# Kernel tuning notes

Hardware: AMD Instinct MI355X
Metric: run time of the kernel (lower is better)

## Reference

```python
import jax, jax.numpy as jnp
import numpy as np

REG_TOPK = 4
REG_CHANNELS = 64
ADD_MEAN = True
TOTAL_DIM = REG_TOPK + (1 if ADD_MEAN else 0)  # 5


def setup_inputs() -> dict:
    key = jax.random.key(0)
    k1, k2, k3 = jax.random.split(key, 3)
    N, C, H, W = 32, 32, 160, 160  # C = 4*(reg_max+1), reg_max=7
    x = jax.random.normal(k1, (N, C, H, W), dtype=jnp.float32)
    # 1x1 conv params, init std=0.01, bias 0 (as in torch module)
    w1 = jax.random.normal(k2, (REG_CHANNELS, 4 * TOTAL_DIM), dtype=jnp.float32) * 0.01
    b1 = jnp.zeros((REG_CHANNELS,), dtype=jnp.float32)
    w2 = jax.random.normal(k3, (1, REG_CHANNELS), dtype=jnp.float32) * 0.01
    b2 = jnp.zeros((1,), dtype=jnp.float32)
    return {"x": x, "w1": w1, "b1": b1, "w2": w2, "b2": b2}


def reference(x, w1, b1, w2, b2):
    N, C, H, W = x.shape
    bins = C // 4
    # softmax over distribution bins; move bins to last axis for top_k
    p = jax.nn.softmax(x.reshape(N, 4, bins, H, W), axis=2)  # (N,4,bins,H,W)
    p = jnp.transpose(p, (0, 1, 3, 4, 2))                    # (N,4,H,W,bins)
    topk, _ = jax.lax.top_k(p, REG_TOPK)                     # (N,4,H,W,k)
    if ADD_MEAN:
        stat = jnp.concatenate([topk, topk.mean(axis=-1, keepdims=True)], axis=-1)
    else:
        stat = topk                                          # (N,4,H,W,total_dim)
    # reshape to (N, 4*total_dim, H, W) matching torch layout (4, total_dim contiguous)
    stat = jnp.transpose(stat, (0, 1, 4, 2, 3)).reshape(N, 4 * TOTAL_DIM, H, W)
    y = jax.nn.relu(jnp.einsum('nchw,oc->nohw', stat, w1) + b1[None, :, None, None])
    y = jax.nn.sigmoid(jnp.einsum('nchw,oc->nohw', y, w2) + b2[None, :, None, None])
    return y
```

## Files before the change

kernel.cpp:

```cpp
#include <hip/hip_runtime.h>

#define HW_ 25600
#define CHW_ (32 * 25600)
#define NPIX 819200
#define ROWH 16

typedef _Float16 f16x8 __attribute__((ext_vector_type(8)));
typedef _Float16 h2 __attribute__((ext_vector_type(2)));
typedef float f32x4 __attribute__((ext_vector_type(4)));

__device__ __forceinline__ unsigned short h2us(_Float16 h) {
    return __builtin_bit_cast(unsigned short, h);
}
__device__ __forceinline__ unsigned packlo(h2 a, h2 b) {
    h2 r = {a.x, b.x};
    return __builtin_bit_cast(unsigned, r);
}
__device__ __forceinline__ unsigned packhi(h2 a, h2 b) {
    h2 r = {a.y, b.y};
    return __builtin_bit_cast(unsigned, r);
}
__device__ __forceinline__ h2 pkrtz(float a, float b) {
    return __builtin_bit_cast(h2, __builtin_amdgcn_cvt_pkrtz(a, b));
}

__global__ __launch_bounds__(256) void dgqp_fused(
    const float* __restrict__ x,
    const float* __restrict__ w1,
    const float* __restrict__ b1,
    const float* __restrict__ w2,
    const float* __restrict__ b2,
    float* __restrict__ out)
{
    __shared__ _Float16 smem[512 * ROWH + 2048];
    _Float16* sstats = smem;
    _Float16* swf    = smem + 512 * ROWH;

    const int tid  = threadIdx.x;
    const int lane = tid & 63;
    const int wpb  = (tid & 192) << 1;
    const int q    = lane & 15;
    const int kg   = lane >> 4;
    const int base = (blockIdx.x * 256 + tid) * 2;
    const unsigned int n = (unsigned int)base / HW_;
    const unsigned int off = (unsigned int)base + n * (unsigned int)(CHW_ - HW_);
    const float* xp = x + off;

    _Float16* row0 = sstats + (tid * 2) * ROWH;
    _Float16* row1 = row0 + ROWH;

#define PROC(g, buf) do {                                                    \
        h2 e[8];                                                             \
        _Pragma("unroll")                                                    \
        for (int b = 0; b < 8; ++b)                                          \
            e[b] = pkrtz(__expf(buf[b].x), __expf(buf[b].y));                \
        h2 t0 = (h2)0, t1 = (h2)0, t2 = (h2)0, t3 = (h2)0;                   \
        _Pragma("unroll")                                                    \
        for (int b = 0; b < 8; ++b) {                                        \
            h2 u0 = __builtin_elementwise_min(t0, e[b]);                     \
            t0    = __builtin_elementwise_max(t0, e[b]);                     \
            h2 u1 = __builtin_elementwise_min(t1, u0);                       \
            t1    = __builtin_elementwise_max(t1, u0);                       \
            h2 u2 = __builtin_elementwise_min(t2, u1);                       \
            t2    = __builtin_elementwise_max(t2, u1);                       \
            t3    = __builtin_elementwise_max(t3, u2);                       \
        }                                                                    \
        h2 sum = ((e[0] + e[1]) + (e[2] + e[3])) + ((e[4] + e[5]) + (e[6] + e[7])); \
        float ix = __builtin_amdgcn_rcpf((float)sum.x);                      \
        float iy = __builtin_amdgcn_rcpf((float)sum.y);                      \
        h2 inv = pkrtz(ix, iy);                                              \
        t0 = t0 * inv; t1 = t1 * inv; t2 = t2 * inv; t3 = t3 * inv;          \
        *reinterpret_cast<uint2*>(row0 + (g) * 4) =                          \
            make_uint2(packlo(t0, t1), packlo(t2, t3));                      \
        *reinterpret_cast<uint2*>(row1 + (g) * 4) =                          \
            make_uint2(packhi(t0, t1), packhi(t2, t3));                      \
    } while (0)

    float2 va[8], vb[8];
    #pragma unroll
    for (int b = 0; b < 8; ++b)
        va[b] = *reinterpret_cast<const float2*>(xp + (size_t)b * HW_);
    #pragma unroll
    for (int b = 0; b < 8; ++b)
        vb[b] = *reinterpret_cast<const float2*>(xp + (size_t)(8 + b) * HW_);
    __builtin_amdgcn_sched_barrier(0);
    PROC(0, va);
    #pragma unroll
    for (int b = 0; b < 8; ++b)
        va[b] = *reinterpret_cast<const float2*>(xp + (size_t)(16 + b) * HW_);
    __builtin_amdgcn_sched_barrier(0);
    PROC(1, vb);
    #pragma unroll
    for (int b = 0; b < 8; ++b)
        vb[b] = *reinterpret_cast<const float2*>(xp + (size_t)(24 + b) * HW_);
    __builtin_amdgcn_sched_barrier(0);
    PROC(2, va);
    __builtin_amdgcn_sched_barrier(0);
    PROC(3, vb);
#undef PROC

    {
        const int col = ((tid >> 6) << 4) | (tid & 15);
        const int kg2 = (tid >> 4) & 3;
        unsigned int pk[4];
        #pragma unroll
        for (int pr = 0; pr < 4; ++pr) {
            unsigned short hh[2];
            #pragma unroll
            for (int e = 0; e < 2; ++e) {
                int k = kg2 * 8 + pr * 2 + e;
                float v = 0.f;
                if (k < 16) {
                    int g = k >> 2, idx = k & 3;
                    v = w1[col * 20 + g * 5 + idx] + 0.25f * w1[col * 20 + g * 5 + 4];
                }
                hh[e] = h2us((_Float16)v);
            }
            pk[pr] = (unsigned int)hh[0] | ((unsigned int)hh[1] << 16);
        }
        *reinterpret_cast<uint4*>(swf + tid * 8) = make_uint4(pk[0], pk[1], pk[2], pk[3]);
    }
    __syncthreads();

    f16x8 wfrag[4];
    #pragma unroll
    for (int ct = 0; ct < 4; ++ct)
        wfrag[ct] = *reinterpret_cast<const f16x8*>(swf + (ct * 64 + lane) * 8);

    f32x4 w2v[4], b1c[4];
    #pragma unroll
    for (int ct = 0; ct < 4; ++ct) {
        w2v[ct] = *reinterpret_cast<const f32x4*>(w2 + ct * 16 + kg * 4);
        b1c[ct] = *reinterpret_cast<const f32x4*>(b1 + ct * 16 + kg * 4);
    }

    const float bb2 = b2[0];
    const int outbase = blockIdx.x * 512 + wpb;

    #pragma unroll
    for (int m = 0; m < 8; ++m) {
        f16x8 sfrag = *reinterpret_cast<const f16x8*>(
            sstats + (wpb + m * 16 + q) * ROWH + kg * 8);

        float pp = 0.f;
        #pragma unroll
        for (int ct = 0; ct < 4; ++ct) {
            f32x4 d = __builtin_amdgcn_mfma_f32_16x16x32_f16(wfrag[ct], sfrag, b1c[ct], 0, 0, 0);
            pp = fmaf(w2v[ct][0], fmaxf(d[0], 0.f), pp);
            pp = fmaf(w2v[ct][1], fmaxf(d[1], 0.f), pp);
            pp = fmaf(w2v[ct][2], fmaxf(d[2], 0.f), pp);
            pp = fmaf(w2v[ct][3], fmaxf(d[3], 0.f), pp);
        }
        pp += __shfl_xor(pp, 16);
        pp += __shfl_xor(pp, 32);
        float y = __builtin_amdgcn_rcpf(1.f + __expf(-(pp + bb2)));
        if (lane < 16)
            out[outbase + m * 16 + q] = y;
    }
}

extern "C" void kernel_launch(void* const* d_in, const int* in_sizes, int n_in,
                              void* d_out, int out_size, void* d_ws, size_t ws_size,
                              hipStream_t stream) {
    const float* x  = (const float*)d_in[0];
    const float* w1 = (const float*)d_in[1];
    const float* b1 = (const float*)d_in[2];
    const float* w2 = (const float*)d_in[3];
    const float* b2 = (const float*)d_in[4];
    float* out = (float*)d_out;

    dgqp_fused<<<NPIX / 512, 256, 0, stream>>>(x, w1, b1, w2, b2, out);
}
```

Before: 29.07 us.

## Process four pixels per thread with float4 loads and halve block size

Each thread now loads float4 (four adjacent pixels) per channel instead of float2, so blocks shrink to 128 threads while still covering 512 pixels. Each wave runs 16 MFMA row tiles instead of 8, and the weight-fragment staging loops twice per thread. The aim is wider, fewer memory transactions and more bytes in flight per thread. The cost is doubled register pressure from the load buffers and fewer waves per block, which may reduce occupancy and latency hiding.

```diff
diff --git a/kernel.cpp b/kernel.cpp
--- a/kernel.cpp
+++ b/kernel.cpp
@@ -24,7 +24,7 @@
     return __builtin_bit_cast(h2, __builtin_amdgcn_cvt_pkrtz(a, b));
 }
 
-__global__ __launch_bounds__(256) void dgqp_fused(
+__global__ __launch_bounds__(128, 4) void dgqp_fused(
     const float* __restrict__ x,
     const float* __restrict__ w1,
     const float* __restrict__ b1,
@@ -38,22 +38,22 @@
 
     const int tid  = threadIdx.x;
     const int lane = tid & 63;
-    const int wpb  = (tid & 192) << 1;
+    const int wv   = tid >> 6;
+    const int wpb  = wv << 8;
     const int q    = lane & 15;
     const int kg   = lane >> 4;
-    const int base = (blockIdx.x * 256 + tid) * 2;
+    const int base = (blockIdx.x * 128 + tid) * 4;
     const unsigned int n = (unsigned int)base / HW_;
     const unsigned int off = (unsigned int)base + n * (unsigned int)(CHW_ - HW_);
     const float* xp = x + off;
 
-    _Float16* row0 = sstats + (tid * 2) * ROWH;
-    _Float16* row1 = row0 + ROWH;
+    _Float16* r0 = sstats + (tid * 4) * ROWH;
 
-#define PROC(g, buf) do {                                                    \
+#define PROCP(g, buf, S0, S1, rA, rB) do {                                   \
         h2 e[8];                                                             \
         _Pragma("unroll")                                                    \
         for (int b = 0; b < 8; ++b)                                          \
-            e[b] = pkrtz(__expf(buf[b].x), __expf(buf[b].y));                \
+            e[b] = pkrtz(__expf(buf[b].S0), __expf(buf[b].S1));              \
         h2 t0 = (h2)0, t1 = (h2)0, t2 = (h2)0, t3 = (h2)0;                   \
         _Pragma("unroll")                                                    \
         for (int b = 0; b < 8; ++b) {                                        \
@@ -70,38 +70,46 @@
         float iy = __builtin_amdgcn_rcpf((float)sum.y);                      \
         h2 inv = pkrtz(ix, iy);                                              \
         t0 = t0 * inv; t1 = t1 * inv; t2 = t2 * inv; t3 = t3 * inv;          \
-        *reinterpret_cast<uint2*>(row0 + (g) * 4) =                          \
+        *reinterpret_cast<uint2*>((rA) + (g) * 4) =                          \
             make_uint2(packlo(t0, t1), packlo(t2, t3));                      \
-        *reinterpret_cast<uint2*>(row1 + (g) * 4) =                          \
+        *reinterpret_cast<uint2*>((rB) + (g) * 4) =                          \
             make_uint2(packhi(t0, t1), packhi(t2, t3));                      \
     } while (0)
 
-    float2 va[8], vb[8];
+#define PROC4(g, buf) do {                                                   \
+        PROCP(g, buf, x, y, r0,            r0 + ROWH);                       \
+        PROCP(g, buf, z, w, r0 + 2 * ROWH, r0 + 3 * ROWH);                   \
+    } while (0)
+
+    float4 va[8], vb[8];
     #pragma unroll
     for (int b = 0; b < 8; ++b)
-        va[b] = *reinterpret_cast<const float2*>(xp + (size_t)b * HW_);
+        va[b] = *reinterpret_cast<const float4*>(xp + (size_t)b * HW_);
     #pragma unroll
     for (int b = 0; b < 8; ++b)
-        vb[b] = *reinterpret_cast<const float2*>(xp + (size_t)(8 + b) * HW_);
+        vb[b] = *reinterpret_cast<const float4*>(xp + (size_t)(8 + b) * HW_);
     __builtin_amdgcn_sched_barrier(0);
-    PROC(0, va);
+    PROC4(0, va);
     #pragma unroll
     for (int b = 0; b < 8; ++b)
-        va[b] = *reinterpret_cast<const float2*>(xp + (size_t)(16 + b) * HW_);
+        va[b] = *reinterpret_cast<const float4*>(xp + (size_t)(16 + b) * HW_);
     __builtin_amdgcn_sched_barrier(0);
-    PROC(1, vb);
+    PROC4(1, vb);
     #pragma unroll
     for (int b = 0; b < 8; ++b)
-        vb[b] = *reinterpret_cast<const float2*>(xp + (size_t)(24 + b) * HW_);
+        vb[b] = *reinterpret_cast<const float4*>(xp + (size_t)(24 + b) * HW_);
     __builtin_amdgcn_sched_barrier(0);
-    PROC(2, va);
+    PROC4(2, va);
     __builtin_amdgcn_sched_barrier(0);
-    PROC(3, vb);
-#undef PROC
+    PROC4(3, vb);
+#undef PROC4
+#undef PROCP
 
-    {
-        const int col = ((tid >> 6) << 4) | (tid & 15);
-        const int kg2 = (tid >> 4) & 3;
+    #pragma unroll
+    for (int sl = 0; sl < 2; ++sl) {
+        const int s   = tid + sl * 128;
+        const int col = ((s >> 6) << 4) | (s & 15);
+        const int kg2 = (s >> 4) & 3;
         unsigned int pk[4];
         #pragma unroll
         for (int pr = 0; pr < 4; ++pr) {
@@ -118,7 +126,7 @@
             }
             pk[pr] = (unsigned int)hh[0] | ((unsigned int)hh[1] << 16);
         }
-        *reinterpret_cast<uint4*>(swf + tid * 8) = make_uint4(pk[0], pk[1], pk[2], pk[3]);
+        *reinterpret_cast<uint4*>(swf + s * 8) = make_uint4(pk[0], pk[1], pk[2], pk[3]);
     }
     __syncthreads();
 
@@ -138,7 +146,7 @@
     const int outbase = blockIdx.x * 512 + wpb;
 
     #pragma unroll
-    for (int m = 0; m < 8; ++m) {
+    for (int m = 0; m < 16; ++m) {
         f16x8 sfrag = *reinterpret_cast<const f16x8*>(
             sstats + (wpb + m * 16 + q) * ROWH + kg * 8);
 
@@ -169,5 +177,5 @@
     const float* b2 = (const float*)d_in[4];
     float* out = (float*)d_out;
 
-    dgqp_fused<<<NPIX / 512, 256, 0, stream>>>(x, w1, b1, w2, b2, out);
+    dgqp_fused<<<NPIX / 512, 128, 0, stream>>>(x, w1, b1, w2, b2, out);
 }
```

Result: slower. 32.43 us (+11.6%).

## Issue all 32 channel loads upfront, pad LDS rows, and set occupancy hint

Applied to the files above, without the earlier changes.

Replaces the double-buffered load/process pipeline with one batch of all 32 float2 channel loads issued before any softmax/top-k work. This maximizes memory-level parallelism per thread. The LDS stats layout changes from 16-half rows per pixel to 40-half rows per pixel pair, padded to avoid bank conflicts on the MFMA fragment reads. Adding a min-blocks-per-CU hint of 4 constrains registers, and holding 64 loaded VGPRs at once raises register pressure and risks spills or lower occupancy.

```diff
diff --git a/kernel.cpp b/kernel.cpp
--- a/kernel.cpp
+++ b/kernel.cpp
@@ -3,7 +3,7 @@
 #define HW_ 25600
 #define CHW_ (32 * 25600)
 #define NPIX 819200
-#define ROWH 16
+#define PROW 40
 
 typedef _Float16 f16x8 __attribute__((ext_vector_type(8)));
 typedef _Float16 h2 __attribute__((ext_vector_type(2)));
@@ -24,7 +24,7 @@
     return __builtin_bit_cast(h2, __builtin_amdgcn_cvt_pkrtz(a, b));
 }
 
-__global__ __launch_bounds__(256) void dgqp_fused(
+__global__ __launch_bounds__(256, 4) void dgqp_fused(
     const float* __restrict__ x,
     const float* __restrict__ w1,
     const float* __restrict__ b1,
@@ -32,9 +32,9 @@
     const float* __restrict__ b2,
     float* __restrict__ out)
 {
-    __shared__ _Float16 smem[512 * ROWH + 2048];
+    __shared__ _Float16 smem[256 * PROW + 2048];
     _Float16* sstats = smem;
-    _Float16* swf    = smem + 512 * ROWH;
+    _Float16* swf    = smem + 256 * PROW;
 
     const int tid  = threadIdx.x;
     const int lane = tid & 63;
@@ -46,14 +46,20 @@
     const unsigned int off = (unsigned int)base + n * (unsigned int)(CHW_ - HW_);
     const float* xp = x + off;
 
-    _Float16* row0 = sstats + (tid * 2) * ROWH;
-    _Float16* row1 = row0 + ROWH;
+    _Float16* row0 = sstats + tid * PROW;
+    _Float16* row1 = row0 + 16;
+
+    float2 v[32];
+    #pragma unroll
+    for (int c = 0; c < 32; ++c)
+        v[c] = *reinterpret_cast<const float2*>(xp + (size_t)c * HW_);
+    __builtin_amdgcn_sched_barrier(0);
 
 #define PROC(g, buf) do {                                                    \
         h2 e[8];                                                             \
         _Pragma("unroll")                                                    \
         for (int b = 0; b < 8; ++b)                                          \
-            e[b] = pkrtz(__expf(buf[b].x), __expf(buf[b].y));                \
+            e[b] = pkrtz(__expf((buf)[b].x), __expf((buf)[b].y));            \
         h2 t0 = (h2)0, t1 = (h2)0, t2 = (h2)0, t3 = (h2)0;                   \
         _Pragma("unroll")                                                    \
         for (int b = 0; b < 8; ++b) {                                        \
@@ -76,27 +82,10 @@
             make_uint2(packhi(t0, t1), packhi(t2, t3));                      \
     } while (0)
 
-    float2 va[8], vb[8];
-    #pragma unroll
-    for (int b = 0; b < 8; ++b)
-        va[b] = *reinterpret_cast<const float2*>(xp + (size_t)b * HW_);
-    #pragma unroll
-    for (int b = 0; b < 8; ++b)
-        vb[b] = *reinterpret_cast<const float2*>(xp + (size_t)(8 + b) * HW_);
-    __builtin_amdgcn_sched_barrier(0);
-    PROC(0, va);
-    #pragma unroll
-    for (int b = 0; b < 8; ++b)
-        va[b] = *reinterpret_cast<const float2*>(xp + (size_t)(16 + b) * HW_);
-    __builtin_amdgcn_sched_barrier(0);
-    PROC(1, vb);
-    #pragma unroll
-    for (int b = 0; b < 8; ++b)
-        vb[b] = *reinterpret_cast<const float2*>(xp + (size_t)(24 + b) * HW_);
-    __builtin_amdgcn_sched_barrier(0);
-    PROC(2, va);
-    __builtin_amdgcn_sched_barrier(0);
-    PROC(3, vb);
+    PROC(0, v + 0);
+    PROC(1, v + 8);
+    PROC(2, v + 16);
+    PROC(3, v + 24);
 #undef PROC
 
     {
@@ -109,12 +98,12 @@
             #pragma unroll
             for (int e = 0; e < 2; ++e) {
                 int k = kg2 * 8 + pr * 2 + e;
-                float v = 0.f;
+                float vv = 0.f;
                 if (k < 16) {
                     int g = k >> 2, idx = k & 3;
-                    v = w1[col * 20 + g * 5 + idx] + 0.25f * w1[col * 20 + g * 5 + 4];
+                    vv = w1[col * 20 + g * 5 + idx] + 0.25f * w1[col * 20 + g * 5 + 4];
                 }
-                hh[e] = h2us((_Float16)v);
+                hh[e] = h2us((_Float16)vv);
             }
             pk[pr] = (unsigned int)hh[0] | ((unsigned int)hh[1] << 16);
         }
@@ -136,11 +125,13 @@
 
     const float bb2 = b2[0];
     const int outbase = blockIdx.x * 512 + wpb;
+    const int qh = q >> 1, qp = q & 1;
 
     #pragma unroll
     for (int m = 0; m < 8; ++m) {
+        const int pairb = (wpb >> 1) + m * 8 + qh;
         f16x8 sfrag = *reinterpret_cast<const f16x8*>(
-            sstats + (wpb + m * 16 + q) * ROWH + kg * 8);
+            sstats + pairb * PROW + qp * 16 + kg * 8);
 
         float pp = 0.f;
         #pragma unroll
```

Result: no change. 29.02 us (-0.2%).
